# Kernel tuning notes

Measured on AMD Instinct MI355X. Metric: run time of the kernel, lower is better.

The kernel has to match this reference:

```python
import jax, jax.numpy as jnp
import numpy as np
import math

B, S, D, H = 4, 2048, 1024, 16
DK = D // H


def setup_inputs() -> dict:
    key = jax.random.key(0)
    k1, k2, k3, k4, k5 = jax.random.split(key, 5)
    inputs = jax.random.normal(k1, (B, S, D), dtype=jnp.float32)
    # additive causal mask: 0 on/below diagonal, -1e9 above
    causal = jnp.triu(jnp.full((S, S), -1e9, dtype=jnp.float32), k=1)
    mask = causal[None, None, :, :]  # [1,1,S,S]
    w_qkv = jax.random.normal(k2, (D, 3 * D), dtype=jnp.float32) * 0.02
    b_qkv = jax.random.normal(k3, (3 * D,), dtype=jnp.float32) * 0.02
    w_head = jax.random.normal(k4, (D, D), dtype=jnp.float32) * 0.02
    b_head = jax.random.normal(k5, (D,), dtype=jnp.float32) * 0.02
    return {"inputs": inputs, "mask": mask, "w_qkv": w_qkv, "b_qkv": b_qkv,
            "w_head": w_head, "b_head": b_head}


def reference(inputs, mask, w_qkv, b_qkv, w_head, b_head):
    # fused QKV projection
    qkv = jnp.einsum('bsd,de->bse', inputs, w_qkv) + b_qkv  # [B,S,3D]
    q, k, v = jnp.split(qkv, 3, axis=-1)
    # split heads -> [B,H,S,DK]
    q = q.reshape(B, S, H, DK).transpose(0, 2, 1, 3)
    k = k.reshape(B, S, H, DK).transpose(0, 2, 1, 3)
    v = v.reshape(B, S, H, DK).transpose(0, 2, 1, 3)
    # scaled dot-product attention with additive mask
    att = jnp.einsum('bhqd,bhkd->bhqk', q, k) / math.sqrt(DK)
    att = att + mask
    att = jax.nn.softmax(att, axis=-1)  # dropout p=0 -> identity
    out = jnp.einsum('bhqk,bhkd->bhqd', att, v)  # [B,H,S,DK]
    # merge heads
    out = out.transpose(0, 2, 1, 3).reshape(B, S, D)
    out = jnp.einsum('bsd,de->bse', out, w_head) + b_head
    return out
```

## Files before the change

### kernel.cpp

```cpp
#include <hip/hip_runtime.h>
#include <stdint.h>

typedef __bf16 bf16x8 __attribute__((ext_vector_type(8)));
typedef float f32x4 __attribute__((ext_vector_type(4)));
typedef float f32x16 __attribute__((ext_vector_type(16)));
typedef unsigned short u16;

#if __has_builtin(__builtin_amdgcn_exp2f)
#define EXP2F(x) __builtin_amdgcn_exp2f(x)
#else
#define EXP2F(x) exp2f(x)
#endif

__device__ __forceinline__ u16 f2bf(float f) {
  union { float f; unsigned u; } v; v.f = f;
  return (u16)((v.u + 0x7fffu + ((v.u >> 16) & 1u)) >> 16);
}

__device__ __forceinline__ unsigned pk2bf(float a, float b) {
  union { __bf16 h[2]; unsigned u; } c;
  c.h[0] = (__bf16)a; c.h[1] = (__bf16)b;
  return c.u;
}

__device__ __forceinline__ f32x16 vz16() {
  f32x16 v;
#pragma unroll
  for (int i = 0; i < 16; ++i) v[i] = 0.f;
  return v;
}

#define GLOAD_LDS16(gp, lp)                                                       \
  __builtin_amdgcn_global_load_lds((__attribute__((address_space(1))) void*)(gp), \
                                   (__attribute__((address_space(3))) void*)(lp), \
                                   16, 0, 0)

__global__ void k_cvt_bf16(const float* __restrict__ in, u16* __restrict__ out, int n4) {
  int i = blockIdx.x * blockDim.x + threadIdx.x;
  if (i >= n4) return;
  float4 v = ((const float4*)in)[i];
  ushort4 o;
  o.x = f2bf(v.x); o.y = f2bf(v.y); o.z = f2bf(v.z); o.w = f2bf(v.w);
  ((ushort4*)out)[i] = o;
}

__global__ void k_transpose_bf16(const float* __restrict__ w, u16* __restrict__ wt,
                                 int K, int N) {
  __shared__ u16 t[32][33];
  int n0 = blockIdx.x * 32, k0 = blockIdx.y * 32;
  int tx = threadIdx.x & 31, ty = threadIdx.x >> 5;
#pragma unroll
  for (int j = 0; j < 4; ++j) {
    int r = ty + j * 8;
    t[r][tx] = f2bf(w[(size_t)(k0 + r) * N + n0 + tx]);
  }
  __syncthreads();
#pragma unroll
  for (int j = 0; j < 4; ++j) {
    int r = ty + j * 8;
    wt[(size_t)(n0 + r) * K + k0 + tx] = t[tx][r];
  }
}

template <int MODE>
__global__ void __launch_bounds__(256, 2)
k_gemm_bt(const u16* __restrict__ A, const u16* __restrict__ Bt,
          const float* __restrict__ bias, u16* __restrict__ outQ,
          u16* __restrict__ outK, u16* __restrict__ outVt,
          float* __restrict__ outF, int Kdim, int Ncols) {
  __shared__ u16 Asq[128 * 64];
  __shared__ u16 Bsq[128 * 64];
  const int tid = threadIdx.x;
  const int lane = tid & 63;
  const int wv = tid >> 6;
  const int g = lane >> 4;
  const int lr = lane & 15;
  const int wr = wv >> 1, wc = wv & 1;
  const int row0 = blockIdx.y * 128;
  const int col0 = blockIdx.x * 128;

  const f32x4 fzero = {0.f, 0.f, 0.f, 0.f};
  f32x4 acc[4][4];
#pragma unroll
  for (int m = 0; m < 4; ++m)
#pragma unroll
    for (int n = 0; n < 4; ++n) acc[m][n] = fzero;

  const u16* Arow = A + (size_t)row0 * Kdim;
  const u16* Brow = Bt + (size_t)col0 * Kdim;

  for (int kt = 0; kt < Kdim; kt += 64) {
#pragma unroll
    for (int j = 0; j < 4; ++j) {
      int unit = j * 256 + wv * 64 + lane;
      int r = unit >> 3, u = unit & 7;
      int ug = u ^ (r & 7);
      GLOAD_LDS16(Arow + (size_t)r * Kdim + kt + ug * 8,
                  &Asq[(size_t)(j * 256 + wv * 64) * 8]);
      GLOAD_LDS16(Brow + (size_t)r * Kdim + kt + ug * 8,
                  &Bsq[(size_t)(j * 256 + wv * 64) * 8]);
    }
    __syncthreads();
#pragma unroll
    for (int kc = 0; kc < 2; ++kc) {
      bf16x8 af[4], bfr[4];
#pragma unroll
      for (int m = 0; m < 4; ++m) {
        int r = wr * 64 + m * 16 + lr;
        int u = (kc * 4 + g) ^ (r & 7);
        af[m] = *(const bf16x8*)((const char*)Asq + r * 128 + u * 16);
      }
#pragma unroll
      for (int n = 0; n < 4; ++n) {
        int r = wc * 64 + n * 16 + lr;
        int u = (kc * 4 + g) ^ (r & 7);
        bfr[n] = *(const bf16x8*)((const char*)Bsq + r * 128 + u * 16);
      }
#pragma unroll
      for (int m = 0; m < 4; ++m)
#pragma unroll
        for (int n = 0; n < 4; ++n)
          acc[m][n] = __builtin_amdgcn_mfma_f32_16x16x32_bf16(af[m], bfr[n],
                                                              acc[m][n], 0, 0, 0);
    }
    __syncthreads();
  }

#pragma unroll
  for (int n = 0; n < 4; ++n) {
    int e = col0 + wc * 64 + n * 16 + lr;
    float bv = bias[e];
    if (MODE == 0) {
      int part = e >> 10;
      int d = e & 1023;
      int hh = d >> 6;
      int dk = d & 63;
#pragma unroll
      for (int m = 0; m < 4; ++m) {
        int tbase = row0 + wr * 64 + m * 16 + g * 4;
        int bb = tbase >> 11;
        int s = tbase & 2047;
        size_t bh = (size_t)((bb << 4) + hh);
        if (part == 2) {
          ushort4 pk;
          pk.x = f2bf(acc[m][n][0] + bv);
          pk.y = f2bf(acc[m][n][1] + bv);
          pk.z = f2bf(acc[m][n][2] + bv);
          pk.w = f2bf(acc[m][n][3] + bv);
          *(ushort4*)(outVt + (bh * 64 + dk) * 2048 + s) = pk;
        } else {
#pragma unroll
          for (int i = 0; i < 4; ++i) {
            float val = acc[m][n][i] + bv;
            size_t off = (bh * 2048 + (size_t)(s + i)) * 64 + dk;
            if (part == 0)
              outQ[off] = f2bf(val * 0.18033688f);
            else
              outK[off] = f2bf(val);
          }
        }
      }
    } else {
#pragma unroll
      for (int m = 0; m < 4; ++m)
#pragma unroll
        for (int i = 0; i < 4; ++i) {
          int t = row0 + wr * 64 + m * 16 + g * 4 + i;
          outF[(size_t)t * Ncols + e] = acc[m][n][i] + bv;
        }
    }
  }
}


__device__ __forceinline__ void stage_kv(const u16* __restrict__ Kb,
                                         const u16* __restrict__ Vb, int kbase,
                                         u16* Kbuf, u16* Vbuf, int wv, int lane) {
#pragma unroll
  for (int j = 0; j < 2; ++j) {
    int unit = j * 256 + wv * 64 + lane;
    int r = unit >> 3, u = unit & 7;
    int ug = u ^ (r & 7);
    GLOAD_LDS16(Kb + (size_t)(kbase + r) * 64 + ug * 8, Kbuf + (j * 256 + wv * 64) * 8);
    GLOAD_LDS16(Vb + (size_t)r * 2048 + kbase + ug * 8, Vbuf + (j * 256 + wv * 64) * 8);
  }
}

__global__ void __launch_bounds__(256, 4)
k_flash(const u16* __restrict__ Qg, const u16* __restrict__ Kg,
        const u16* __restrict__ Vtg, u16* __restrict__ attn) {
  __shared__ u16 KV[2][2][4096];
  const int tid = threadIdx.x;
  const int lane = tid & 63;
  const int wv = tid >> 6;
  const int ql = lane & 31;
  const int hi = lane >> 5;

  const int bid = blockIdx.x;
  const int n_lo = bid & 3;
  const int bh = (bid >> 2) & 63;
  const int n_hi = bid >> 8;
  const int qb = 4 * ((n_lo + n_hi) & 3) + ((n_lo + 2 * n_hi) & 3);

  const u16* Qb = Qg + (size_t)bh * 2048 * 64;
  const u16* Kb = Kg + (size_t)bh * 2048 * 64;
  const u16* Vb = Vtg + (size_t)bh * 64 * 2048;
  const int bb = bh >> 4, hh = bh & 15;

  int off[4];
#pragma unroll
  for (int j = 0; j < 4; ++j) off[j] = ql * 64 + (((2 * j + hi) ^ (ql & 7)) * 8);

  const int ntile = 2 * qb + 2;
  const int q0w = qb * 128 + wv * 32;
  const int q = q0w + ql;

  bf16x8 qf[4];
#pragma unroll
  for (int ds = 0; ds < 4; ++ds)
    qf[ds] = *(const bf16x8*)(Qb + (size_t)q * 64 + ds * 16 + hi * 8);

  f32x16 o0 = vz16(), o1 = vz16();
  float mrow = -1e30f, lrow = 0.f;

  stage_kv(Kb, Vb, 0, &KV[0][0][0], &KV[0][1][0], wv, lane);
  __syncthreads();

  for (int kt = 0; kt < ntile; ++kt) {
    const int kbase = kt * 64;
    const int nb = kt & 1;
    if (kt + 1 < ntile)
      stage_kv(Kb, Vb, kbase + 64, &KV[nb ^ 1][0][0], &KV[nb ^ 1][1][0], wv, lane);
    const u16* Kbuf = &KV[nb][0][0];
    const u16* Vbuf = &KV[nb][1][0];

    if (kbase <= q0w + 31) {
      const bool need1 = (kbase + 32) <= (q0w + 31);
      f32x16 s0 = vz16(), s1 = vz16();
      __builtin_amdgcn_s_setprio(1);
#pragma unroll
      for (int ds = 0; ds < 4; ++ds) {
        bf16x8 kf = *(const bf16x8*)(Kbuf + off[ds]);
        s0 = __builtin_amdgcn_mfma_f32_32x32x16_bf16(kf, qf[ds], s0, 0, 0, 0);
      }
      if (need1) {
#pragma unroll
        for (int ds = 0; ds < 4; ++ds) {
          bf16x8 kf = *(const bf16x8*)(Kbuf + 2048 + off[ds]);
          s1 = __builtin_amdgcn_mfma_f32_32x32x16_bf16(kf, qf[ds], s1, 0, 0, 0);
        }
      }
      __builtin_amdgcn_s_setprio(0);

      if (kbase + 63 > q0w) {
#pragma unroll
        for (int r = 0; r < 16; ++r) {
          const int krel = (r & 3) + 8 * (r >> 2) + 4 * hi;
          if (kbase + krel > q) s0[r] = -1e30f;
          if (kbase + 32 + krel > q) s1[r] = -1e30f;
        }
      }

      float a0[8];
#pragma unroll
      for (int i = 0; i < 8; ++i)
        a0[i] = fmaxf(fmaxf(s0[i], s0[i + 8]), fmaxf(s1[i], s1[i + 8]));
      float a1[4];
#pragma unroll
      for (int i = 0; i < 4; ++i) a1[i] = fmaxf(a0[i], a0[i + 4]);
      float tm = fmaxf(fmaxf(a1[0], a1[1]), fmaxf(a1[2], a1[3]));
      tm = fmaxf(tm, __shfl_xor(tm, 32));

      if (!__all(tm - mrow <= 11.5417f)) {
        float mn = fmaxf(mrow, tm);
        float al = EXP2F(mrow - mn);
        mrow = mn;
        lrow *= al;
        o0 *= al;
        o1 *= al;
      }

#pragma unroll
      for (int r = 0; r < 16; ++r) {
        s0[r] = EXP2F(s0[r] - mrow);
        s1[r] = EXP2F(s1[r] - mrow);
      }
      float b0[8];
#pragma unroll
      for (int i = 0; i < 8; ++i) b0[i] = (s0[i] + s0[i + 8]) + (s1[i] + s1[i + 8]);
      float b1[4];
#pragma unroll
      for (int i = 0; i < 4; ++i) b1[i] = b0[i] + b0[i + 4];
      float rs = (b1[0] + b1[1]) + (b1[2] + b1[3]);
      rs += __shfl_xor(rs, 32);
      lrow += rs;

      unsigned W[4][4];
#pragma unroll
      for (int kc = 0; kc < 4; ++kc) {
        if (kc < 2 || need1) {
          const int h2 = kc & 1;
          float v0 = (kc < 2) ? s0[8 * h2 + 0] : s1[8 * h2 + 0];
          float v1 = (kc < 2) ? s0[8 * h2 + 1] : s1[8 * h2 + 1];
          float v2 = (kc < 2) ? s0[8 * h2 + 2] : s1[8 * h2 + 2];
          float v3 = (kc < 2) ? s0[8 * h2 + 3] : s1[8 * h2 + 3];
          float v4 = (kc < 2) ? s0[8 * h2 + 4] : s1[8 * h2 + 4];
          float v5 = (kc < 2) ? s0[8 * h2 + 5] : s1[8 * h2 + 5];
          float v6 = (kc < 2) ? s0[8 * h2 + 6] : s1[8 * h2 + 6];
          float v7 = (kc < 2) ? s0[8 * h2 + 7] : s1[8 * h2 + 7];
          unsigned w0 = pk2bf(v0, v1), w1 = pk2bf(v2, v3);
          unsigned w2 = pk2bf(v4, v5), w3 = pk2bf(v6, v7);
          unsigned pw0 = (unsigned)__shfl_xor((int)w0, 32);
          unsigned pw1 = (unsigned)__shfl_xor((int)w1, 32);
          unsigned pw2 = (unsigned)__shfl_xor((int)w2, 32);
          unsigned pw3 = (unsigned)__shfl_xor((int)w3, 32);
          W[kc][0] = hi ? pw2 : w0;
          W[kc][1] = hi ? pw3 : w1;
          W[kc][2] = hi ? w2 : pw0;
          W[kc][3] = hi ? w3 : pw1;
        }
      }

      __builtin_amdgcn_s_setprio(1);
#pragma unroll
      for (int kc = 0; kc < 4; ++kc) {
        if (kc < 2 || need1) {
          union { unsigned u[4]; bf16x8 v; } pf;
          pf.u[0] = W[kc][0]; pf.u[1] = W[kc][1];
          pf.u[2] = W[kc][2]; pf.u[3] = W[kc][3];
          bf16x8 vf0 = *(const bf16x8*)(Vbuf + off[kc]);
          o0 = __builtin_amdgcn_mfma_f32_32x32x16_bf16(vf0, pf.v, o0, 0, 0, 0);
          bf16x8 vf1 = *(const bf16x8*)(Vbuf + 2048 + off[kc]);
          o1 = __builtin_amdgcn_mfma_f32_32x32x16_bf16(vf1, pf.v, o1, 0, 0, 0);
        }
      }
      __builtin_amdgcn_s_setprio(0);
    }
    __syncthreads();
  }

  const float inv = 1.f / lrow;
  const size_t rowoff = ((size_t)(bb * 2048 + q)) * 1024 + hh * 64;
#pragma unroll
  for (int r4 = 0; r4 < 4; ++r4) {
    ushort4 pa;
    pa.x = f2bf(o0[4 * r4 + 0] * inv);
    pa.y = f2bf(o0[4 * r4 + 1] * inv);
    pa.z = f2bf(o0[4 * r4 + 2] * inv);
    pa.w = f2bf(o0[4 * r4 + 3] * inv);
    *(ushort4*)(attn + rowoff + 8 * r4 + 4 * hi) = pa;
    ushort4 pb;
    pb.x = f2bf(o1[4 * r4 + 0] * inv);
    pb.y = f2bf(o1[4 * r4 + 1] * inv);
    pb.z = f2bf(o1[4 * r4 + 2] * inv);
    pb.w = f2bf(o1[4 * r4 + 3] * inv);
    *(ushort4*)(attn + rowoff + 32 + 8 * r4 + 4 * hi) = pb;
  }
}

extern "C" void kernel_launch(void* const* d_in, const int* in_sizes, int n_in,
                              void* d_out, int out_size, void* d_ws, size_t ws_size,
                              hipStream_t stream) {
  const float* x      = (const float*)d_in[0];
  const float* w_qkv  = (const float*)d_in[2];
  const float* b_qkv  = (const float*)d_in[3];
  const float* w_head = (const float*)d_in[4];
  const float* b_head = (const float*)d_in[5];
  float* out = (float*)d_out;

  u16* Xb    = (u16*)d_ws;
  u16* Wqkvt = Xb + (size_t)8192 * 1024;
  u16* Wht   = Wqkvt + (size_t)3072 * 1024;
  u16* Qw    = Wht + (size_t)1024 * 1024;
  u16* Kw    = Qw + (size_t)64 * 2048 * 64;
  u16* Vtw   = Kw + (size_t)64 * 2048 * 64;
  u16* Attn  = Xb;

  k_cvt_bf16<<<8192, 256, 0, stream>>>(x, Xb, (8192 * 1024) / 4);
  k_transpose_bf16<<<dim3(96, 32), 256, 0, stream>>>(w_qkv, Wqkvt, 1024, 3072);
  k_transpose_bf16<<<dim3(32, 32), 256, 0, stream>>>(w_head, Wht, 1024, 1024);
  k_gemm_bt<0><<<dim3(24, 64), 256, 0, stream>>>(Xb, Wqkvt, b_qkv, Qw, Kw, Vtw,
                                                 nullptr, 1024, 3072);
  k_flash<<<1024, 256, 0, stream>>>(Qw, Kw, Vtw, Attn);
  k_gemm_bt<1><<<dim3(8, 64), 256, 0, stream>>>(Attn, Wht, b_head, nullptr, nullptr,
                                                nullptr, out, 1024, 1024);
}
```

Before: 160.2 us.

## Split long causal query blocks across two KV ranges with a combine pass

The flash-attention grid grows from 1024 to 1536 blocks. Each of the eight longest query blocks per head is split into two halves of its key range, which evens out the causal work per block and shortens the tail. Each half writes fp32 partial outputs plus its row max and sum into scratch space reused from the output and weight buffers. A new combine kernel merges the two halves with rescaling before the head projection. The cost is an extra launch and an fp32 round-trip of the partials, and the code relies on the scratch buffers being free at that point.

```diff
diff --git a/kernel.cpp b/kernel.cpp
--- a/kernel.cpp
+++ b/kernel.cpp
@@ -188,7 +188,8 @@
 
 __global__ void __launch_bounds__(256, 4)
 k_flash(const u16* __restrict__ Qg, const u16* __restrict__ Kg,
-        const u16* __restrict__ Vtg, u16* __restrict__ attn) {
+        const u16* __restrict__ Vtg, u16* __restrict__ attn,
+        float* __restrict__ outP, float* __restrict__ mlb) {
   __shared__ u16 KV[2][2][4096];
   const int tid = threadIdx.x;
   const int lane = tid & 63;
@@ -196,11 +197,18 @@
   const int ql = lane & 31;
   const int hi = lane >> 5;
 
+  const int T_QB[24] = {15,15,7, 14,14, 13,13,6, 12,12, 11,11,5, 10,10, 9,9,4, 8,8, 3,2,1,0};
+  const int T_KS[24] = { 0,16,0,  0,15,  0,14,0,  0,13,  0,12,0,  0,11, 0,10,0, 0,9, 0,0,0,0};
+  const int T_KC[24] = {16,16,16,15,15, 14,14,14, 13,13, 12,12,12,11,11,10,10,10,9,9, 8,6,4,2};
+  const int T_MD[24] = { 1, 2,0,  1, 2,  1, 2,0,  1, 2,  1, 2,0,  1, 2, 1, 2,0, 1,2, 0,0,0,0};
+
   const int bid = blockIdx.x;
-  const int n_lo = bid & 3;
-  const int bh = (bid >> 2) & 63;
-  const int n_hi = bid >> 8;
-  const int qb = 4 * ((n_lo + n_hi) & 3) + ((n_lo + 2 * n_hi) & 3);
+  const int g2 = bid >> 6;
+  const int bh = bid & 63;
+  const int qb = T_QB[g2];
+  const int ks = T_KS[g2];
+  const int kcnt = T_KC[g2];
+  const int md = T_MD[g2];
 
   const u16* Qb = Qg + (size_t)bh * 2048 * 64;
   const u16* Kb = Kg + (size_t)bh * 2048 * 64;
@@ -211,7 +219,6 @@
 #pragma unroll
   for (int j = 0; j < 4; ++j) off[j] = ql * 64 + (((2 * j + hi) ^ (ql & 7)) * 8);
 
-  const int ntile = 2 * qb + 2;
   const int q0w = qb * 128 + wv * 32;
   const int q = q0w + ql;
 
@@ -223,13 +230,13 @@
   f32x16 o0 = vz16(), o1 = vz16();
   float mrow = -1e30f, lrow = 0.f;
 
-  stage_kv(Kb, Vb, 0, &KV[0][0][0], &KV[0][1][0], wv, lane);
+  stage_kv(Kb, Vb, ks * 64, &KV[0][0][0], &KV[0][1][0], wv, lane);
   __syncthreads();
 
-  for (int kt = 0; kt < ntile; ++kt) {
-    const int kbase = kt * 64;
-    const int nb = kt & 1;
-    if (kt + 1 < ntile)
+  for (int it = 0; it < kcnt; ++it) {
+    const int kbase = (ks + it) * 64;
+    const int nb = it & 1;
+    if (it + 1 < kcnt)
       stage_kv(Kb, Vb, kbase + 64, &KV[nb ^ 1][0][0], &KV[nb ^ 1][1][0], wv, lane);
     const u16* Kbuf = &KV[nb][0][0];
     const u16* Vbuf = &KV[nb][1][0];
@@ -339,22 +346,67 @@
     __syncthreads();
   }
 
-  const float inv = 1.f / lrow;
-  const size_t rowoff = ((size_t)(bb * 2048 + q)) * 1024 + hh * 64;
-#pragma unroll
-  for (int r4 = 0; r4 < 4; ++r4) {
-    ushort4 pa;
-    pa.x = f2bf(o0[4 * r4 + 0] * inv);
-    pa.y = f2bf(o0[4 * r4 + 1] * inv);
-    pa.z = f2bf(o0[4 * r4 + 2] * inv);
-    pa.w = f2bf(o0[4 * r4 + 3] * inv);
-    *(ushort4*)(attn + rowoff + 8 * r4 + 4 * hi) = pa;
-    ushort4 pb;
-    pb.x = f2bf(o1[4 * r4 + 0] * inv);
-    pb.y = f2bf(o1[4 * r4 + 1] * inv);
-    pb.z = f2bf(o1[4 * r4 + 2] * inv);
-    pb.w = f2bf(o1[4 * r4 + 3] * inv);
-    *(ushort4*)(attn + rowoff + 32 + 8 * r4 + 4 * hi) = pb;
+  if (md == 0) {
+    const float inv = 1.f / lrow;
+    const size_t rowoff = ((size_t)(bb * 2048 + q)) * 1024 + hh * 64;
+#pragma unroll
+    for (int r4 = 0; r4 < 4; ++r4) {
+      ushort4 pa;
+      pa.x = f2bf(o0[4 * r4 + 0] * inv);
+      pa.y = f2bf(o0[4 * r4 + 1] * inv);
+      pa.z = f2bf(o0[4 * r4 + 2] * inv);
+      pa.w = f2bf(o0[4 * r4 + 3] * inv);
+      *(ushort4*)(attn + rowoff + 8 * r4 + 4 * hi) = pa;
+      ushort4 pb;
+      pb.x = f2bf(o1[4 * r4 + 0] * inv);
+      pb.y = f2bf(o1[4 * r4 + 1] * inv);
+      pb.z = f2bf(o1[4 * r4 + 2] * inv);
+      pb.w = f2bf(o1[4 * r4 + 3] * inv);
+      *(ushort4*)(attn + rowoff + 32 + 8 * r4 + 4 * hi) = pb;
+    }
+  } else {
+    const int pidx = bh * 8 + (qb - 8);
+    const int r = wv * 32 + ql;
+    float* Op = outP + ((md == 1) ? 0 : 4194304) + (size_t)pidx * 8192 + r * 64;
+#pragma unroll
+    for (int r4 = 0; r4 < 4; ++r4) {
+      float4 pa = {o0[4 * r4 + 0], o0[4 * r4 + 1], o0[4 * r4 + 2], o0[4 * r4 + 3]};
+      *(float4*)(Op + 8 * r4 + 4 * hi) = pa;
+      float4 pb = {o1[4 * r4 + 0], o1[4 * r4 + 1], o1[4 * r4 + 2], o1[4 * r4 + 3]};
+      *(float4*)(Op + 32 + 8 * r4 + 4 * hi) = pb;
+    }
+    if (hi == 0) {
+      float* mlp = mlb + (size_t)pidx * 512 + r * 4 + ((md == 1) ? 0 : 2);
+      mlp[0] = lrow;
+      mlp[1] = mrow;
+    }
+  }
+}
+
+__global__ void k_combine(const float* __restrict__ Op, const float* __restrict__ mlb,
+                          u16* __restrict__ attn) {
+  const int pidx = blockIdx.x;
+  const int bh = pidx >> 3, qb = 8 + (pidx & 7);
+  const int bb = bh >> 4, hh = bh & 15;
+  const int tid = threadIdx.x;
+  const int dq = (tid & 15) * 4;
+  const float* O0 = Op + (size_t)pidx * 8192;
+  const float* O1 = O0 + 4194304;
+  for (int rb = 0; rb < 128; rb += 16) {
+    const int r = rb + (tid >> 4);
+    const float* ml = mlb + (size_t)pidx * 512 + r * 4;
+    float l0 = ml[0], m0 = ml[1], l1 = ml[2], m1 = ml[3];
+    float m = fmaxf(m0, m1);
+    float a0 = EXP2F(m0 - m), a1 = EXP2F(m1 - m);
+    float inv = 1.f / (a0 * l0 + a1 * l1);
+    float4 x0 = *(const float4*)(O0 + r * 64 + dq);
+    float4 x1 = *(const float4*)(O1 + r * 64 + dq);
+    ushort4 o;
+    o.x = f2bf((a0 * x0.x + a1 * x1.x) * inv);
+    o.y = f2bf((a0 * x0.y + a1 * x1.y) * inv);
+    o.z = f2bf((a0 * x0.z + a1 * x1.z) * inv);
+    o.w = f2bf((a0 * x0.w + a1 * x1.w) * inv);
+    *(ushort4*)(attn + ((size_t)(bb * 2048 + qb * 128 + r)) * 1024 + hh * 64 + dq) = o;
   }
 }
 
@@ -375,13 +427,16 @@
   u16* Kw    = Qw + (size_t)64 * 2048 * 64;
   u16* Vtw   = Kw + (size_t)64 * 2048 * 64;
   u16* Attn  = Xb;
+  float* Opart = out;
+  float* Mlb   = (float*)Wqkvt;
 
   k_cvt_bf16<<<8192, 256, 0, stream>>>(x, Xb, (8192 * 1024) / 4);
   k_transpose_bf16<<<dim3(96, 32), 256, 0, stream>>>(w_qkv, Wqkvt, 1024, 3072);
   k_transpose_bf16<<<dim3(32, 32), 256, 0, stream>>>(w_head, Wht, 1024, 1024);
   k_gemm_bt<0><<<dim3(24, 64), 256, 0, stream>>>(Xb, Wqkvt, b_qkv, Qw, Kw, Vtw,
                                                  nullptr, 1024, 3072);
-  k_flash<<<1024, 256, 0, stream>>>(Qw, Kw, Vtw, Attn);
+  k_flash<<<1536, 256, 0, stream>>>(Qw, Kw, Vtw, Attn, Opart, Mlb);
+  k_combine<<<512, 256, 0, stream>>>(Opart, Mlb, Attn);
   k_gemm_bt<1><<<dim3(8, 64), 256, 0, stream>>>(Attn, Wht, b_head, nullptr, nullptr,
                                                 nullptr, out, 1024, 1024);
 }
```

New measurement: 163.6 us. 1.02x slower.
